# Kernel optimization log

Measured on AMD Instinct MI355X. Metric: run time of the kernel, lower is better.

## Reference

```python
import jax, jax.numpy as jnp
import numpy as np

IN_F = 128
OUT_F = 64
ALPHA = 0.2  # LeakyReLU slope for attention logits
NEG_INF = -9e15


def setup_inputs() -> dict:
    key = jax.random.key(0)
    k1, k2, k3, k4 = jax.random.split(key, 4)
    B, N = 4, 2048
    h = jax.random.normal(k1, (B, N, IN_F), dtype=jnp.float32)
    adj = jax.random.randint(k2, (B, N, N), 0, 2, dtype=jnp.int32)
    # xavier_uniform with gain=1.414
    def xavier(k, shape, gain=1.414):
        fan_in, fan_out = shape[0], shape[1]
        bound = gain * np.sqrt(6.0 / (fan_in + fan_out))
        return jax.random.uniform(k, shape, jnp.float32, -bound, bound)
    W = xavier(k3, (IN_F, OUT_F))
    a = xavier(k4, (2 * OUT_F, 1))
    return {"h": h, "adj": adj, "W": W, "a": a}


def reference(h, adj, W, a):
    # Wh: [B, N, F_out]
    Wh = jnp.einsum("bnf,fo->bno", h, W)
    # e_ij = LeakyReLU(a_left . Wh_i + a_right . Wh_j), avoiding the
    # O(N^2 * 2F) concatenated tensor the torch code materializes.
    a_l = a[:OUT_F, 0]   # [F_out]
    a_r = a[OUT_F:, 0]   # [F_out]
    e_l = Wh @ a_l       # [B, N]
    e_r = Wh @ a_r       # [B, N]
    e = jax.nn.leaky_relu(e_l[:, :, None] + e_r[:, None, :], ALPHA)  # [B,N,N]
    masked = jnp.where(adj > 0, e, NEG_INF)
    attention = jax.nn.softmax(masked, axis=2)
    # dropout p=0.0 (eval-mode / deterministic) -> identity
    h_prime = jax.nn.leaky_relu(jnp.einsum("bij,bjo->bio", attention, Wh), 0.01)
    return (h_prime, attention)
```

## Files before the change

### kernel.cpp

```cpp
#include <hip/hip_runtime.h>

#define NN 2048
#define BB 4
#define IN_F 128
#define OUT_F 64

typedef __attribute__((ext_vector_type(8))) short short8;
typedef __attribute__((ext_vector_type(4))) float f32x4;
typedef __attribute__((ext_vector_type(4))) int i32x4;

__device__ __forceinline__ ushort f2bf(float f) {
  uint u = __float_as_uint(f);
  uint r = (u + 0x7fffu + ((u >> 16) & 1u)) >> 16;
  return (ushort)r;
}
__device__ __forceinline__ float bf2f(ushort s) {
  return __uint_as_float(((uint)s) << 16);
}

__global__ __launch_bounds__(64) void wh_el_er_kernel(
    const float* __restrict__ h, const float* __restrict__ W,
    const float* __restrict__ a, ushort* __restrict__ Whbf,
    float* __restrict__ el, float* __restrict__ er) {
  int row = blockIdx.x;
  int o = threadIdx.x;
  const float* hr = h + (size_t)row * IN_F;
  float wh = 0.f;
  #pragma unroll 8
  for (int f = 0; f < IN_F; ++f) wh += hr[f] * W[f * OUT_F + o];
  Whbf[(size_t)row * OUT_F + o] = f2bf(wh);
  float vl = wh * a[o];
  float vr = wh * a[OUT_F + o];
  #pragma unroll
  for (int d = 32; d > 0; d >>= 1) {
    vl += __shfl_down(vl, d);
    vr += __shfl_down(vr, d);
  }
  if (o == 0) { el[row] = vl; er[row] = vr; }
}

__global__ __launch_bounds__(256) void transpose_kernel(
    const ushort* __restrict__ Whbf, ushort* __restrict__ WhbfT) {
  __shared__ uint tile[64][65];
  int b = blockIdx.x >> 5;
  int j0 = (blockIdx.x & 31) << 6;
  int t = threadIdx.x;
  int o = t & 63, jg = t >> 6;
  #pragma unroll
  for (int m = 0; m < 16; ++m) {
    int jj = jg * 16 + m;
    tile[jj][o] = (uint)Whbf[((size_t)(b * NN + j0 + jj)) * OUT_F + o];
  }
  __syncthreads();
  int oo = t >> 2, grp = t & 3;
  uint out[8];
  #pragma unroll
  for (int m = 0; m < 16; m += 2) {
    uint u0 = tile[grp * 16 + m][oo];
    uint u1 = tile[grp * 16 + m + 1][oo];
    out[m >> 1] = u0 | (u1 << 16);
  }
  uint4* dst = (uint4*)(WhbfT + ((size_t)(b * OUT_F + oo)) * NN + j0 + grp * 16);
  dst[0] = *(uint4*)&out[0];
  dst[1] = *(uint4*)&out[4];
}

__global__ __launch_bounds__(512, 8) void attn_kernel(
    const int* __restrict__ adj, const ushort* __restrict__ WhbfT,
    const float* __restrict__ el, const float* __restrict__ er,
    float* __restrict__ attn_out, float* __restrict__ hprime) {
  __shared__ __align__(16) char pbuf[8 * 4096];
  __shared__ float red[4][16][17];
  __shared__ float sinv[8];

  int blk = blockIdx.x;
  int b = blk >> 8;
  int i0 = (blk & 255) << 3;
  int tid = threadIdx.x;
  int w = tid >> 6, lane = tid & 63;

  int i = i0 + w;
  float eli = el[(size_t)b * NN + i];
  const i32x4* arow4 = (const i32x4*)(adj + ((size_t)(b * NN + i)) * NN);
  const f32x4* er4 = (const f32x4*)(er + (size_t)b * NN);

  uint2 pva[8];
  float ssum = 0.f;
  #pragma unroll
  for (int it = 0; it < 8; ++it) {
    i32x4 av = arow4[lane + 64 * it];
    f32x4 ev = er4[lane + 64 * it];
    float pe[4];
    float evv[4] = {ev.x, ev.y, ev.z, ev.w};
    int   avv[4] = {av.x, av.y, av.z, av.w};
    #pragma unroll
    for (int k = 0; k < 4; ++k) {
      float e = eli + evv[k];
      e = e > 0.f ? e : 0.2f * e;
      float x = __expf(e);
      pe[k] = avv[k] > 0 ? x : 0.f;
      ssum += pe[k];
    }
    uint2 w2;
    w2.x = (uint)f2bf(pe[0]) | ((uint)f2bf(pe[1]) << 16);
    w2.y = (uint)f2bf(pe[2]) | ((uint)f2bf(pe[3]) << 16);
    pva[it] = w2;
  }
  #pragma unroll
  for (int d = 32; d > 0; d >>= 1) ssum += __shfl_xor(ssum, d);
  float inv = 1.f / ssum;
  if (lane == 0) sinv[w] = inv;

  char* prow = pbuf + w * 4096;
  int sw = w << 4;
  #pragma unroll
  for (int it = 0; it < 8; ++it)
    *(uint2*)(prow + (((lane + 64 * it) * 8) ^ sw)) = pva[it];
  __syncthreads();

  {
    float* orow = attn_out + ((size_t)(b * NN + i)) * NN;
    #pragma unroll
    for (int it = 0; it < 8; ++it) {
      uint2 w2 = pva[it];
      f32x4 v;
      v.x = bf2f((ushort)(w2.x & 0xffff)) * inv;
      v.y = bf2f((ushort)(w2.x >> 16)) * inv;
      v.z = bf2f((ushort)(w2.y & 0xffff)) * inv;
      v.w = bf2f((ushort)(w2.y >> 16)) * inv;
      __builtin_nontemporal_store(v, (f32x4*)(orow + (lane + 64 * it) * 4));
    }
  }

  int ntile = w >> 1, khalf = w & 1;
  int o0 = ntile * 16;
  int lo16 = lane & 15, hi4 = lane >> 4;

  const char* prowA = pbuf + (lo16 & 7) * 4096;
  int swA = (lo16 & 7) << 4;
  const ushort* brow = WhbfT + ((size_t)(b * OUT_F + o0 + lo16)) * NN;
  short8 zero8 = {0, 0, 0, 0, 0, 0, 0, 0};

  f32x4 acc = {0.f, 0.f, 0.f, 0.f};
  #pragma unroll 4
  for (int kk = 0; kk < 32; ++kk) {
    int kbase = khalf * 1024 + kk * 32 + hi4 * 8;
    short8 afrag = *(const short8*)(prowA + ((kbase * 2) ^ swA));
    afrag = lo16 < 8 ? afrag : zero8;
    short8 bfrag = *(const short8*)(brow + kbase);
    acc = __builtin_amdgcn_mfma_f32_16x16x32_bf16(afrag, bfrag, acc, 0, 0, 0);
  }

  if (khalf == 1) {
    #pragma unroll
    for (int q = 0; q < 4; ++q) red[ntile][hi4 * 4 + q][lo16] = acc[q];
  }
  __syncthreads();
  if (khalf == 0 && hi4 < 2) {
    #pragma unroll
    for (int q = 0; q < 4; ++q) {
      int crow = hi4 * 4 + q;
      float v = (acc[q] + red[ntile][crow][lo16]) * sinv[crow];
      v = v > 0.f ? v : 0.01f * v;
      hprime[((size_t)(b * NN + i0 + crow)) * OUT_F + o0 + lo16] = v;
    }
  }
}

extern "C" void kernel_launch(void* const* d_in, const int* in_sizes, int n_in,
                              void* d_out, int out_size, void* d_ws, size_t ws_size,
                              hipStream_t stream) {
  const float* h  = (const float*)d_in[0];
  const int* adj  = (const int*)d_in[1];
  const float* W  = (const float*)d_in[2];
  const float* a  = (const float*)d_in[3];

  float* hprime   = (float*)d_out;
  float* attn_out = (float*)d_out + (size_t)BB * NN * OUT_F;

  ushort* Whbf  = (ushort*)d_ws;
  ushort* WhbfT = Whbf + (size_t)BB * NN * OUT_F;
  float* el = (float*)(WhbfT + (size_t)BB * OUT_F * NN);
  float* er = el + (size_t)BB * NN;

  hipLaunchKernelGGL(wh_el_er_kernel, dim3(BB * NN), dim3(64), 0, stream,
                     h, W, a, Whbf, el, er);
  hipLaunchKernelGGL(transpose_kernel, dim3(BB * (NN / 64)), dim3(256), 0, stream,
                     Whbf, WhbfT);
  hipLaunchKernelGGL(attn_kernel, dim3(BB * (NN / 8)), dim3(512), 0, stream,
                     adj, WhbfT, el, er, attn_out, hprime);
}
```

Before: 61.48 us.

## Split attention into softmax and PV kernels with 16-row MFMA tiles

Splits the fused attention kernel in two. A softmax kernel writes unnormalized bf16 probabilities into the first half of each attn_out row and stores the per-row inverse sum. A PV kernel then reads those back, processes 16 rows per block so the 16x16 MFMA tile is fully used instead of half-zeroed, writes the normalized fp32 attention in place, and computes h_prime. This removes the wasted MFMA lanes but adds an extra global round trip of the bf16 probability buffer and a fourth kernel launch.

```diff
diff --git a/kernel.cpp b/kernel.cpp
--- a/kernel.cpp
+++ b/kernel.cpp
@@ -65,24 +65,16 @@
   dst[1] = *(uint4*)&out[4];
 }
 
-__global__ __launch_bounds__(512, 8) void attn_kernel(
-    const int* __restrict__ adj, const ushort* __restrict__ WhbfT,
-    const float* __restrict__ el, const float* __restrict__ er,
-    float* __restrict__ attn_out, float* __restrict__ hprime) {
-  __shared__ __align__(16) char pbuf[8 * 4096];
-  __shared__ float red[4][16][17];
-  __shared__ float sinv[8];
-
-  int blk = blockIdx.x;
-  int b = blk >> 8;
-  int i0 = (blk & 255) << 3;
-  int tid = threadIdx.x;
-  int w = tid >> 6, lane = tid & 63;
-
-  int i = i0 + w;
-  float eli = el[(size_t)b * NN + i];
-  const i32x4* arow4 = (const i32x4*)(adj + ((size_t)(b * NN + i)) * NN);
-  const f32x4* er4 = (const f32x4*)(er + (size_t)b * NN);
+__global__ __launch_bounds__(256) void softmax_kernel(
+    const int* __restrict__ adj, const float* __restrict__ el,
+    const float* __restrict__ er, float* __restrict__ attn_out,
+    float* __restrict__ sinv) {
+  int lane = threadIdx.x & 63;
+  int row = blockIdx.x * 4 + (threadIdx.x >> 6);
+  int b = row >> 11;
+  float eli = el[row];
+  const i32x4* arow4 = (const i32x4*)(adj + (size_t)row * NN);
+  const f32x4* er4 = (const f32x4*)(er + ((size_t)b << 11));
 
   uint2 pva[8];
   float ssum = 0.f;
@@ -90,13 +82,13 @@
   for (int it = 0; it < 8; ++it) {
     i32x4 av = arow4[lane + 64 * it];
     f32x4 ev = er4[lane + 64 * it];
-    float pe[4];
     float evv[4] = {ev.x, ev.y, ev.z, ev.w};
     int   avv[4] = {av.x, av.y, av.z, av.w};
+    float pe[4];
     #pragma unroll
     for (int k = 0; k < 4; ++k) {
       float e = eli + evv[k];
-      e = e > 0.f ? e : 0.2f * e;
+      e = fmaxf(e, 0.2f * e);
       float x = __expf(e);
       pe[k] = avv[k] > 0 ? x : 0.f;
       ssum += pe[k];
@@ -108,45 +100,83 @@
   }
   #pragma unroll
   for (int d = 32; d > 0; d >>= 1) ssum += __shfl_xor(ssum, d);
-  float inv = 1.f / ssum;
-  if (lane == 0) sinv[w] = inv;
-
-  char* prow = pbuf + w * 4096;
-  int sw = w << 4;
+
+  ushort* prow = (ushort*)(attn_out + (size_t)row * NN);
   #pragma unroll
   for (int it = 0; it < 8; ++it)
-    *(uint2*)(prow + (((lane + 64 * it) * 8) ^ sw)) = pva[it];
+    *(uint2*)(prow + (lane + 64 * it) * 4) = pva[it];
+  if (lane == 0) sinv[row] = 1.f / ssum;
+}
+
+__global__ __launch_bounds__(512, 4) void pv_kernel(
+    const ushort* __restrict__ WhbfT, const float* __restrict__ sinv,
+    float* __restrict__ attn_out, float* __restrict__ hprime) {
+  __shared__ __align__(16) char pbuf[16 * 4096];
+  __shared__ float red[4][16][17];
+
+  int blk = blockIdx.x;
+  int b = blk >> 7;
+  int i0 = (blk & 127) << 4;
+  int tid = threadIdx.x;
+  int wave = tid >> 6, lane = tid & 63;
+
+  int r0 = wave * 2, r1 = r0 + 1;
+  int ga = b * NN + i0 + r0, gb = b * NN + i0 + r1;
+
+  const ushort* pr0 = (const ushort*)(attn_out + (size_t)ga * NN);
+  const ushort* pr1 = (const ushort*)(attn_out + (size_t)gb * NN);
+  uint2 pva0[8], pva1[8];
+  #pragma unroll
+  for (int it = 0; it < 8; ++it) {
+    pva0[it] = *(const uint2*)(pr0 + (lane + 64 * it) * 4);
+    pva1[it] = *(const uint2*)(pr1 + (lane + 64 * it) * 4);
+  }
+  {
+    char* lr0 = pbuf + r0 * 4096;
+    char* lr1 = pbuf + r1 * 4096;
+    int sw0 = (r0 & 7) << 4, sw1 = (r1 & 7) << 4;
+    #pragma unroll
+    for (int it = 0; it < 8; ++it) {
+      *(uint2*)(lr0 + (((lane + 64 * it) * 8) ^ sw0)) = pva0[it];
+      *(uint2*)(lr1 + (((lane + 64 * it) * 8) ^ sw1)) = pva1[it];
+    }
+  }
   __syncthreads();
 
   {
-    float* orow = attn_out + ((size_t)(b * NN + i)) * NN;
+    float inv0 = sinv[ga], inv1 = sinv[gb];
+    f32x4* or0 = (f32x4*)(attn_out + (size_t)ga * NN);
+    f32x4* or1 = (f32x4*)(attn_out + (size_t)gb * NN);
     #pragma unroll
     for (int it = 0; it < 8; ++it) {
-      uint2 w2 = pva[it];
-      f32x4 v;
-      v.x = bf2f((ushort)(w2.x & 0xffff)) * inv;
-      v.y = bf2f((ushort)(w2.x >> 16)) * inv;
-      v.z = bf2f((ushort)(w2.y & 0xffff)) * inv;
-      v.w = bf2f((ushort)(w2.y >> 16)) * inv;
-      __builtin_nontemporal_store(v, (f32x4*)(orow + (lane + 64 * it) * 4));
-    }
-  }
-
-  int ntile = w >> 1, khalf = w & 1;
+      uint2 w0 = pva0[it], w1 = pva1[it];
+      f32x4 v0, v1;
+      v0.x = bf2f((ushort)(w0.x & 0xffff)) * inv0;
+      v0.y = bf2f((ushort)(w0.x >> 16)) * inv0;
+      v0.z = bf2f((ushort)(w0.y & 0xffff)) * inv0;
+      v0.w = bf2f((ushort)(w0.y >> 16)) * inv0;
+      or0[lane + 64 * it] = v0;
+      v1.x = bf2f((ushort)(w1.x & 0xffff)) * inv1;
+      v1.y = bf2f((ushort)(w1.x >> 16)) * inv1;
+      v1.z = bf2f((ushort)(w1.y & 0xffff)) * inv1;
+      v1.w = bf2f((ushort)(w1.y >> 16)) * inv1;
+      or1[lane + 64 * it] = v1;
+    }
+  }
+
+  int ntile = wave >> 1, khalf = wave & 1;
   int o0 = ntile * 16;
   int lo16 = lane & 15, hi4 = lane >> 4;
 
-  const char* prowA = pbuf + (lo16 & 7) * 4096;
+  const char* prowA = pbuf + lo16 * 4096;
   int swA = (lo16 & 7) << 4;
   const ushort* brow = WhbfT + ((size_t)(b * OUT_F + o0 + lo16)) * NN;
-  short8 zero8 = {0, 0, 0, 0, 0, 0, 0, 0};
 
   f32x4 acc = {0.f, 0.f, 0.f, 0.f};
   #pragma unroll 4
   for (int kk = 0; kk < 32; ++kk) {
     int kbase = khalf * 1024 + kk * 32 + hi4 * 8;
     short8 afrag = *(const short8*)(prowA + ((kbase * 2) ^ swA));
-    afrag = lo16 < 8 ? afrag : zero8;
     short8 bfrag = *(const short8*)(brow + kbase);
     acc = __builtin_amdgcn_mfma_f32_16x16x32_bf16(afrag, bfrag, acc, 0, 0, 0);
   }
@@ -156,11 +186,11 @@
     for (int q = 0; q < 4; ++q) red[ntile][hi4 * 4 + q][lo16] = acc[q];
   }
   __syncthreads();
-  if (khalf == 0 && hi4 < 2) {
+  if (khalf == 0) {
     #pragma unroll
     for (int q = 0; q < 4; ++q) {
       int crow = hi4 * 4 + q;
-      float v = (acc[q] + red[ntile][crow][lo16]) * sinv[crow];
+      float v = (acc[q] + red[ntile][crow][lo16]) * sinv[b * NN + i0 + crow];
       v = v > 0.f ? v : 0.01f * v;
       hprime[((size_t)(b * NN + i0 + crow)) * OUT_F + o0 + lo16] = v;
     }
@@ -182,11 +212,14 @@
   ushort* WhbfT = Whbf + (size_t)BB * NN * OUT_F;
   float* el = (float*)(WhbfT + (size_t)BB * OUT_F * NN);
   float* er = el + (size_t)BB * NN;
+  float* sinv = er + (size_t)BB * NN;
 
   hipLaunchKernelGGL(wh_el_er_kernel, dim3(BB * NN), dim3(64), 0, stream,
                      h, W, a, Whbf, el, er);
   hipLaunchKernelGGL(transpose_kernel, dim3(BB * (NN / 64)), dim3(256), 0, stream,
                      Whbf, WhbfT);
-  hipLaunchKernelGGL(attn_kernel, dim3(BB * (NN / 8)), dim3(512), 0, stream,
-                     adj, WhbfT, el, er, attn_out, hprime);
-}
+  hipLaunchKernelGGL(softmax_kernel, dim3(BB * NN / 4), dim3(256), 0, stream,
+                     adj, el, er, attn_out, sinv);
+  hipLaunchKernelGGL(pv_kernel, dim3(BB * (NN / 16)), dim3(512), 0, stream,
+                     WhbfT, sinv, attn_out, hprime);
+}
```

New measurement: 63.03 us. +2.5%, slower.
